# Optimization experiments

Hardware: AMD Instinct MI355X
Metric: run time of the kernel (lower is better)

## Reference

```python
import jax, jax.numpy as jnp
import numpy as np

NUM_EMBEDDINGS = 1024
EMBEDDING_DIM = 64


def setup_inputs() -> dict:
    key = jax.random.key(0)
    kx, kw = jax.random.split(key)
    x = jax.random.normal(kx, (16, 4096, EMBEDDING_DIM), dtype=jnp.float32)
    # torch init: uniform(-1/K, 1/K)
    bound = 1.0 / NUM_EMBEDDINGS
    weight = jax.random.uniform(kw, (NUM_EMBEDDINGS, EMBEDDING_DIM),
                                dtype=jnp.float32, minval=-bound, maxval=bound)
    return {"x": x, "weight": weight}


def reference(x, weight):
    flat_x = x.reshape(-1, EMBEDDING_DIM)                      # [N, D]
    x_sq = jnp.sum(flat_x ** 2, axis=1, keepdims=True)
    w_sq = jnp.sum(weight ** 2, axis=1)[None, :]
    distances = x_sq - 2.0 * (flat_x @ weight.T) + w_sq
    encoding_indices = jnp.argmin(distances, axis=1)           # [N]
    quantized = weight[encoding_indices]                       # [N, D]
    e_latent_loss = jnp.mean((jax.lax.stop_gradient(quantized) - flat_x) ** 2)
    q_latent_loss = jnp.mean((quantized - jax.lax.stop_gradient(flat_x)) ** 2)
    loss = q_latent_loss + 0.25 * e_latent_loss
    # straight-through estimator
    quantized = flat_x + jax.lax.stop_gradient(quantized - flat_x)
    return quantized.reshape(x.shape), encoding_indices, loss
```

## Files before the change

kernel.cpp:

```cpp
#include <hip/hip_runtime.h>
#include <math.h>

#define EMB_D 64
#define MARGIN 6.0e-5f

typedef float  f32x4  __attribute__((ext_vector_type(4)));
typedef short  bf16x8 __attribute__((ext_vector_type(8)));

__device__ __forceinline__ unsigned short f2bf(float f) {
    unsigned int u = __float_as_uint(f);
    return (unsigned short)((u + 0x7FFFu + ((u >> 16) & 1u)) >> 16);
}
__device__ __forceinline__ float bf2f(unsigned short h) {
    return __uint_as_float(((unsigned int)h) << 16);
}

union Pack8 { ushort u[8]; bf16x8 v; uint4 q; };

__device__ __forceinline__ bf16x8 ldbf8(const unsigned short* p) {
    union { uint4 u; bf16x8 v; } c;
    c.u = *(const uint4*)p;
    return c.v;
}

__global__ __launch_bounds__(256)
void vq_prepw_kernel(const float* __restrict__ w,
                     unsigned short* __restrict__ wt_hi,
                     unsigned short* __restrict__ wt_lo,
                     float* __restrict__ wsq, float* __restrict__ loss_out,
                     int K) {
    const int i = blockIdx.x * 256 + threadIdx.x;
    if (i == 0) loss_out[0] = 0.f;
    if (i >= K * 8) return;
    const int krow = i >> 3, q = i & 7;
    const int dest = ((krow >> 6) << 9) + (((krow >> 4) & 3) << 7) + (q << 4)
                   + (krow & 15);
    const float* src = w + (size_t)krow * EMB_D + q * 8;
    Pack8 h, l;
#pragma unroll
    for (int j = 0; j < 8; ++j) {
        const float f = src[j];
        h.u[j] = f2bf(f);
        l.u[j] = f2bf(f - bf2f(h.u[j]));
    }
    ((uint4*)wt_hi)[dest] = h.q;
    ((uint4*)wt_lo)[dest] = l.q;

    if (i < K) {
        const float* wr = w + (size_t)i * EMB_D;
        float r[8];
#pragma unroll
        for (int j = 0; j < 8; ++j) r[j] = __fmul_rn(wr[j], wr[j]);
#pragma unroll
        for (int t = 1; t < 8; ++t)
#pragma unroll
            for (int j = 0; j < 8; ++j)
                r[j] = __fadd_rn(r[j], __fmul_rn(wr[t * 8 + j], wr[t * 8 + j]));
        float a = __fadd_rn(__fadd_rn(r[0], r[1]), __fadd_rn(r[2], r[3]));
        float b = __fadd_rn(__fadd_rn(r[4], r[5]), __fadd_rn(r[6], r[7]));
        wsq[i] = __fadd_rn(a, b);
    }
}

__global__ __launch_bounds__(256, 4)
void vq_screen_kernel(const float* __restrict__ x,
                      const unsigned short* __restrict__ wt_hi,
                      const unsigned short* __restrict__ wt_lo,
                      const float* __restrict__ wsq, int* __restrict__ fidx,
                      int* __restrict__ status, int* __restrict__ k2arr,
                      int K, int N) {
    const int tid  = threadIdx.x;
    const int lane = tid & 63;
    const int wave = tid >> 6;
    const int quad = lane >> 4;
    const int c16  = lane & 15;
    const int rowbase = blockIdx.x * 64 + wave * 16;

    __shared__ uint4 sh4[512];
    __shared__ uint4 sl4[512];
    __shared__ float wsq_lds[1024];
    __shared__ float M1[4][16][17], M2[4][16][17];
    __shared__ int   N1[4][16][17], N2[4][16][17];

    const float* xrow = x + (size_t)(rowbase + c16) * EMB_D + quad * 8;
    Pack8 ah0, al0, ah1, al1;
#pragma unroll
    for (int j = 0; j < 8; ++j) {
        const float f0 = xrow[j];
        ah0.u[j] = f2bf(f0); al0.u[j] = f2bf(f0 - bf2f(ah0.u[j]));
        const float f1 = xrow[32 + j];
        ah1.u[j] = f2bf(f1); al1.u[j] = f2bf(f1 - bf2f(ah1.u[j]));
    }
    const bf16x8 ahi0 = ah0.v, alo0 = al0.v, ahi1 = ah1.v, alo1 = al1.v;

    ((float4*)wsq_lds)[tid] = ((const float4*)wsq)[tid];

    float s1[4], s2[4];
    int   k1[4], k2[4];
#pragma unroll
    for (int i = 0; i < 4; ++i) {
        s1[i] = INFINITY; s2[i] = INFINITY; k1[i] = 0; k2[i] = 0;
    }

    const uint4* gh = (const uint4*)wt_hi;
    const uint4* gl = (const uint4*)wt_lo;
    uint4 ph0 = gh[tid], ph1 = gh[256 + tid];
    uint4 pl0 = gl[tid], pl1 = gl[256 + tid];

    const int nseg = K >> 6;
    for (int seg = 0; seg < nseg; ++seg) {
        sh4[tid] = ph0; sh4[256 + tid] = ph1;
        sl4[tid] = pl0; sl4[256 + tid] = pl1;
        __syncthreads();
        if (seg + 1 < nseg) {
            const int b = (seg + 1) * 512;
            ph0 = gh[b + tid]; ph1 = gh[b + 256 + tid];
            pl0 = gl[b + tid]; pl1 = gl[b + 256 + tid];
        }

#pragma unroll
        for (int s = 0; s < 4; ++s) {
            const unsigned short* shp = (const unsigned short*)sh4;
            const unsigned short* slp = (const unsigned short*)sl4;
            const bf16x8 bhi0 = ldbf8(shp + (s * 128 + lane) * 8);
            const bf16x8 bhi1 = ldbf8(shp + (s * 128 + 64 + lane) * 8);
            const bf16x8 blo0 = ldbf8(slp + (s * 128 + lane) * 8);
            const bf16x8 blo1 = ldbf8(slp + (s * 128 + 64 + lane) * 8);

            f32x4 acc0 = {0.f, 0.f, 0.f, 0.f};
            f32x4 acc1 = {0.f, 0.f, 0.f, 0.f};
            acc0 = __builtin_amdgcn_mfma_f32_16x16x32_bf16(alo0, bhi0, acc0, 0, 0, 0);
            acc1 = __builtin_amdgcn_mfma_f32_16x16x32_bf16(alo1, bhi1, acc1, 0, 0, 0);
            acc0 = __builtin_amdgcn_mfma_f32_16x16x32_bf16(ahi0, blo0, acc0, 0, 0, 0);
            acc1 = __builtin_amdgcn_mfma_f32_16x16x32_bf16(ahi1, blo1, acc1, 0, 0, 0);
            acc0 = __builtin_amdgcn_mfma_f32_16x16x32_bf16(ahi0, bhi0, acc0, 0, 0, 0);
            acc1 = __builtin_amdgcn_mfma_f32_16x16x32_bf16(ahi1, bhi1, acc1, 0, 0, 0);

            const int   kk = seg * 64 + s * 16 + c16;
            const float wq = wsq_lds[kk];
#pragma unroll
            for (int i = 0; i < 4; ++i) {
                const float sc = fmaf(-2.0f, acc0[i] + acc1[i], wq);
                const bool c1 = sc < s1[i];
                const bool c2 = sc < s2[i];
                k2[i] = c1 ? k1[i] : (c2 ? kk : k2[i]);
                k1[i] = c1 ? kk : k1[i];
                s2[i] = __builtin_amdgcn_fmed3f(sc, s1[i], s2[i]);
                s1[i] = fminf(sc, s1[i]);
            }
        }
        __syncthreads();
    }

#pragma unroll
    for (int i = 0; i < 4; ++i) {
        const int r16 = quad * 4 + i;
        M1[wave][r16][c16] = s1[i];  N1[wave][r16][c16] = k1[i];
        M2[wave][r16][c16] = s2[i];  N2[wave][r16][c16] = k2[i];
    }
    __syncthreads();
    if (lane < 16) {
        float g1 = INFINITY, g2 = INFINITY, g3 = INFINITY;
        int   gk1 = 0, gk2 = 0;
#pragma unroll
        for (int c = 0; c < 16; ++c) {
#pragma unroll
            for (int h = 0; h < 2; ++h) {
                const float s = h == 0 ? M1[wave][lane][c] : M2[wave][lane][c];
                const int   k = h == 0 ? N1[wave][lane][c] : N2[wave][lane][c];
                if (s < g1)      { g3 = g2; g2 = g1; gk2 = gk1; g1 = s; gk1 = k; }
                else if (s < g2) { g3 = g2; g2 = s; gk2 = k; }
                else if (s < g3) { g3 = s; }
            }
        }
        const int row = rowbase + lane;
        fidx[row] = gk1;
        int st = 0;
        if (g2 - g1 <= MARGIN) st = (g3 - g1 > MARGIN) ? 1 : 2;
        status[row] = st;
        if (st == 1) k2arr[row] = gk2;
    }
}

__global__ __launch_bounds__(256)
void vq_gather_kernel(const float* __restrict__ x, const float* __restrict__ w,
                      const float* __restrict__ wsq, const int* __restrict__ fidx,
                      const int* __restrict__ status, const int* __restrict__ k2arr,
                      float* __restrict__ out, float* __restrict__ loss_out,
                      int N, int K, float scale) {
    const int tid  = threadIdx.x;
    const int lane = tid & 63;
    const int wave = tid >> 6;
    __shared__ int kf[64];
    __shared__ int strow[64];
    if (tid < 64) {
        const int row = blockIdx.x * 64 + tid;
        kf[tid]    = fidx[row];
        strow[tid] = status[row];
    }
    __syncthreads();

    if (tid < 64 && strow[tid] == 1) {
        const int row = blockIdx.x * 64 + tid;
        const int ka = kf[tid], kb = k2arr[row];
        const float4* xp = (const float4*)(x + (size_t)row * EMB_D);
        const float4* wa = (const float4*)(w + (size_t)ka * EMB_D);
        const float4* wb = (const float4*)(w + (size_t)kb * EMB_D);
        float r[8];
        double aa0 = 0, aa1 = 0, aa2 = 0, aa3 = 0;
        double ab0 = 0, ab1 = 0, ab2 = 0, ab3 = 0;
#pragma unroll
        for (int q = 0; q < 16; ++q) {
            const float4 xv = xp[q], va = wa[q], vb = wb[q];
            const int j = (q & 1) * 4;
            if (q < 2) {
                r[j + 0] = __fmul_rn(xv.x, xv.x);
                r[j + 1] = __fmul_rn(xv.y, xv.y);
                r[j + 2] = __fmul_rn(xv.z, xv.z);
                r[j + 3] = __fmul_rn(xv.w, xv.w);
            } else {
                r[j + 0] = __fadd_rn(r[j + 0], __fmul_rn(xv.x, xv.x));
                r[j + 1] = __fadd_rn(r[j + 1], __fmul_rn(xv.y, xv.y));
                r[j + 2] = __fadd_rn(r[j + 2], __fmul_rn(xv.z, xv.z));
                r[j + 3] = __fadd_rn(r[j + 3], __fmul_rn(xv.w, xv.w));
            }
            aa0 = fma((double)xv.x, (double)va.x, aa0);
            aa1 = fma((double)xv.y, (double)va.y, aa1);
            aa2 = fma((double)xv.z, (double)va.z, aa2);
            aa3 = fma((double)xv.w, (double)va.w, aa3);
            ab0 = fma((double)xv.x, (double)vb.x, ab0);
            ab1 = fma((double)xv.y, (double)vb.y, ab1);
            ab2 = fma((double)xv.z, (double)vb.z, ab2);
            ab3 = fma((double)xv.w, (double)vb.w, ab3);
        }
        const float xsq = __fadd_rn(
            __fadd_rn(__fadd_rn(r[0], r[1]), __fadd_rn(r[2], r[3])),
            __fadd_rn(__fadd_rn(r[4], r[5]), __fadd_rn(r[6], r[7])));
        const float mfa = (float)((aa0 + aa1) + (aa2 + aa3));
        const float mfb = (float)((ab0 + ab1) + (ab2 + ab3));
        const float sa = __fadd_rn(__fsub_rn(xsq, __fmul_rn(2.0f, mfa)), wsq[ka]);
        const float sb = __fadd_rn(__fsub_rn(xsq, __fmul_rn(2.0f, mfb)), wsq[kb]);
        int win = ka;
        if (sb < sa || (sb == sa && kb < ka)) win = kb;
        kf[tid] = win;
    }
    __syncthreads();

    __shared__ float4 xs4[16];
    __shared__ float  xsqs;
    __shared__ float  ls[256];
    __shared__ int    lk[256];
    for (int i = 0; i < 64; ++i) {
        if (strow[i] != 2) continue;
        const int row = blockIdx.x * 64 + i;
        if (tid < 16) xs4[tid] = ((const float4*)(x + (size_t)row * EMB_D))[tid];
        __syncthreads();
        if (tid == 0) {
            const float* xf = (const float*)xs4;
            float r[8];
#pragma unroll
            for (int j = 0; j < 8; ++j) r[j] = __fmul_rn(xf[j], xf[j]);
#pragma unroll
            for (int t = 1; t < 8; ++t)
#pragma unroll
                for (int j = 0; j < 8; ++j)
                    r[j] = __fadd_rn(r[j], __fmul_rn(xf[t * 8 + j], xf[t * 8 + j]));
            xsqs = __fadd_rn(
                __fadd_rn(__fadd_rn(r[0], r[1]), __fadd_rn(r[2], r[3])),
                __fadd_rn(__fadd_rn(r[4], r[5]), __fadd_rn(r[6], r[7])));
        }
        __syncthreads();
        const float xsq = xsqs;

        float bs = INFINITY;
        int   bk = K;
        for (int t = 0; t < 4; ++t) {
            const int k = wave * (K >> 2) + t * 64 + lane;
            const float4* wr4 = (const float4*)(w + (size_t)k * EMB_D);
            double a0 = 0.0, a1 = 0.0, a2 = 0.0, a3 = 0.0;
#pragma unroll
            for (int q = 0; q < EMB_D / 4; ++q) {
                const float4 xv = xs4[q];
                const float4 wv = wr4[q];
                a0 = fma((double)xv.x, (double)wv.x, a0);
                a1 = fma((double)xv.y, (double)wv.y, a1);
                a2 = fma((double)xv.z, (double)wv.z, a2);
                a3 = fma((double)xv.w, (double)wv.w, a3);
            }
            const float mf = (float)((a0 + a1) + (a2 + a3));
            const float t2 = __fsub_rn(xsq, __fmul_rn(2.0f, mf));
            const float sc = __fadd_rn(t2, wsq[k]);
            if (sc < bs || (sc == bs && k < bk)) { bs = sc; bk = k; }
        }
        ls[tid] = bs; lk[tid] = bk;
        __syncthreads();
        if (wave == 0) {
            float gs = ls[lane];
            int   gk = lk[lane];
#pragma unroll
            for (int c = 1; c < 4; ++c) {
                const float os = ls[c * 64 + lane];
                const int   ok = lk[c * 64 + lane];
                if (os < gs || (os == gs && ok < gk)) { gs = os; gk = ok; }
            }
#pragma unroll
            for (int off = 32; off > 0; off >>= 1) {
                const float os = __shfl_down(gs, off);
                const int   ok = __shfl_down(gk, off);
                if (os < gs || (os == gs && ok < gk)) { gs = os; gk = ok; }
            }
            if (lane == 0) kf[i] = gk;
        }
        __syncthreads();
    }

    if (tid < 64) {
        const int row = blockIdx.x * 64 + tid;
        out[(size_t)N * EMB_D + row] = (float)kf[tid];
    }
    float lpart = 0.f;
#pragma unroll
    for (int rep = 0; rep < 4; ++rep) {
        int f4   = rep * 256 + tid;
        int rr   = f4 >> 4;
        int c    = f4 & 15;
        int k    = kf[rr];
        int grow = blockIdx.x * 64 + rr;
        float4 wv = ((const float4*)(w + (size_t)k * EMB_D))[c];
        float4 xq = ((const float4*)(x + (size_t)grow * EMB_D))[c];
        ((float4*)out)[(size_t)grow * (EMB_D / 4) + c] = wv;
        float dx = wv.x - xq.x, dy = wv.y - xq.y;
        float dz = wv.z - xq.z, dw = wv.w - xq.w;
        lpart += dx * dx + dy * dy + dz * dz + dw * dw;
    }
#pragma unroll
    for (int off = 32; off > 0; off >>= 1) lpart += __shfl_down(lpart, off);
    __shared__ float lred[4];
    if (lane == 0) lred[wave] = lpart;
    __syncthreads();
    if (tid == 0)
        atomicAdd(loss_out, ((lred[0] + lred[1]) + (lred[2] + lred[3])) * scale);
}

extern "C" void kernel_launch(void* const* d_in, const int* in_sizes, int n_in,
                              void* d_out, int out_size, void* d_ws, size_t ws_size,
                              hipStream_t stream) {
    const float* x = (const float*)d_in[0];
    const float* w = (const float*)d_in[1];
    float* out = (float*)d_out;
    const int xsz = in_sizes[0];
    const int wsz = in_sizes[1];
    const int N   = xsz / EMB_D;
    const int K   = wsz / EMB_D;
    const int NB  = N / 64;
    float* loss_out = out + (size_t)N * EMB_D + N;

    int*   status = (int*)d_ws;
    int*   k2arr  = status + N;
    int*   fidx   = k2arr + N;
    float* wsq    = (float*)(fidx + N);
    unsigned short* wt_hi = (unsigned short*)(wsq + K);
    unsigned short* wt_lo = wt_hi + (size_t)K * EMB_D;

    vq_prepw_kernel<<<(K * 8 + 255) / 256, 256, 0, stream>>>(w, wt_hi, wt_lo,
                                                             wsq, loss_out, K);
    vq_screen_kernel<<<NB, 256, 0, stream>>>(x, wt_hi, wt_lo, wsq, fidx,
                                             status, k2arr, K, N);
    vq_gather_kernel<<<NB, 256, 0, stream>>>(x, w, wsq, fidx, status, k2arr,
                                             out, loss_out, N, K,
                                             1.25f / (float)xsz);
}
```

Measured before the change: 147.6 us.

## Fuse screen and gather kernels and pack score plus index into one key

Merges the screening and gather kernels into one kernel, so fidx/status/k2 are passed through shared memory and no longer round-trip through global memory, and one launch is removed. The top-2 tracking now packs a positively-offset score (with its low 10 mantissa bits truncated) together with the code index into a single unsigned key and uses integer min/max. This shortens the per-candidate compare-select chain. The truncation costs score precision, and the tie margin is widened to compensate. The key trick assumes K≤1024 and that the offset scores are positive.

```diff
diff --git a/kernel.cpp b/kernel.cpp
--- a/kernel.cpp
+++ b/kernel.cpp
@@ -2,7 +2,7 @@
 #include <math.h>
 
 #define EMB_D 64
-#define MARGIN 6.0e-5f
+#define MARGIN 1.0e-4f
 
 typedef float  f32x4  __attribute__((ext_vector_type(4)));
 typedef short  bf16x8 __attribute__((ext_vector_type(8)));
@@ -14,9 +14,7 @@
 __device__ __forceinline__ float bf2f(unsigned short h) {
     return __uint_as_float(((unsigned int)h) << 16);
 }
-
 union Pack8 { ushort u[8]; bf16x8 v; uint4 q; };
-
 __device__ __forceinline__ bf16x8 ldbf8(const unsigned short* p) {
     union { uint4 u; bf16x8 v; } c;
     c.u = *(const uint4*)p;
@@ -63,12 +61,11 @@
 }
 
 __global__ __launch_bounds__(256, 4)
-void vq_screen_kernel(const float* __restrict__ x,
-                      const unsigned short* __restrict__ wt_hi,
-                      const unsigned short* __restrict__ wt_lo,
-                      const float* __restrict__ wsq, int* __restrict__ fidx,
-                      int* __restrict__ status, int* __restrict__ k2arr,
-                      int K, int N) {
+void vq_mega_kernel(const float* __restrict__ x, const float* __restrict__ w,
+                    const unsigned short* __restrict__ wt_hi,
+                    const unsigned short* __restrict__ wt_lo,
+                    const float* __restrict__ wsq, float* __restrict__ out,
+                    float* __restrict__ loss_out, int K, int N, float scale) {
     const int tid  = threadIdx.x;
     const int lane = tid & 63;
     const int wave = tid >> 6;
@@ -78,9 +75,9 @@
 
     __shared__ uint4 sh4[512];
     __shared__ uint4 sl4[512];
-    __shared__ float wsq_lds[1024];
-    __shared__ float M1[4][16][17], M2[4][16][17];
-    __shared__ int   N1[4][16][17], N2[4][16][17];
+    __shared__ float wsqo[1024];
+    __shared__ unsigned int U1[4][16][17], U2[4][16][17];
+    __shared__ int kf[64], strow[64], k2s[64];
 
     const float* xrow = x + (size_t)(rowbase + c16) * EMB_D + quad * 8;
     Pack8 ah0, al0, ah1, al1;
@@ -93,14 +90,15 @@
     }
     const bf16x8 ahi0 = ah0.v, alo0 = al0.v, ahi1 = ah1.v, alo1 = al1.v;
 
-    ((float4*)wsq_lds)[tid] = ((const float4*)wsq)[tid];
-
-    float s1[4], s2[4];
-    int   k1[4], k2[4];
-#pragma unroll
-    for (int i = 0; i < 4; ++i) {
-        s1[i] = INFINITY; s2[i] = INFINITY; k1[i] = 0; k2[i] = 0;
-    }
+    {
+        float4 v = ((const float4*)wsq)[tid];
+        v.x += 0.25f; v.y += 0.25f; v.z += 0.25f; v.w += 0.25f;
+        ((float4*)wsqo)[tid] = v;
+    }
+
+    unsigned int u1[4], u2[4];
+#pragma unroll
+    for (int i = 0; i < 4; ++i) { u1[i] = 0xFFFFFFFFu; u2[i] = 0xFFFFFFFFu; }
 
     const uint4* gh = (const uint4*)wt_hi;
     const uint4* gl = (const uint4*)wt_lo;
@@ -117,11 +115,11 @@
             ph0 = gh[b + tid]; ph1 = gh[b + 256 + tid];
             pl0 = gl[b + tid]; pl1 = gl[b + 256 + tid];
         }
+        const unsigned short* shp = (const unsigned short*)sh4;
+        const unsigned short* slp = (const unsigned short*)sl4;
 
 #pragma unroll
         for (int s = 0; s < 4; ++s) {
-            const unsigned short* shp = (const unsigned short*)sh4;
-            const unsigned short* slp = (const unsigned short*)sl4;
             const bf16x8 bhi0 = ldbf8(shp + (s * 128 + lane) * 8);
             const bf16x8 bhi1 = ldbf8(shp + (s * 128 + 64 + lane) * 8);
             const bf16x8 blo0 = ldbf8(slp + (s * 128 + lane) * 8);
@@ -136,17 +134,16 @@
             acc0 = __builtin_amdgcn_mfma_f32_16x16x32_bf16(ahi0, bhi0, acc0, 0, 0, 0);
             acc1 = __builtin_amdgcn_mfma_f32_16x16x32_bf16(ahi1, bhi1, acc1, 0, 0, 0);
 
-            const int   kk = seg * 64 + s * 16 + c16;
-            const float wq = wsq_lds[kk];
+            const int   kk  = seg * 64 + s * 16 + c16;
+            const float wqo = wsqo[kk];
 #pragma unroll
             for (int i = 0; i < 4; ++i) {
-                const float sc = fmaf(-2.0f, acc0[i] + acc1[i], wq);
-                const bool c1 = sc < s1[i];
-                const bool c2 = sc < s2[i];
-                k2[i] = c1 ? k1[i] : (c2 ? kk : k2[i]);
-                k1[i] = c1 ? kk : k1[i];
-                s2[i] = __builtin_amdgcn_fmed3f(sc, s1[i], s2[i]);
-                s1[i] = fminf(sc, s1[i]);
+                const float sp  = fmaf(-2.0f, acc0[i] + acc1[i], wqo);
+                const unsigned int key =
+                    (__float_as_uint(sp) & 0xFFFFFC00u) | (unsigned int)kk;
+                const unsigned int mx = u1[i] > key ? u1[i] : key;
+                u1[i] = u1[i] < key ? u1[i] : key;
+                u2[i] = u2[i] < mx  ? u2[i] : mx;
             }
         }
         __syncthreads();
@@ -155,54 +152,42 @@
 #pragma unroll
     for (int i = 0; i < 4; ++i) {
         const int r16 = quad * 4 + i;
-        M1[wave][r16][c16] = s1[i];  N1[wave][r16][c16] = k1[i];
-        M2[wave][r16][c16] = s2[i];  N2[wave][r16][c16] = k2[i];
+        U1[wave][r16][c16] = u1[i];
+        U2[wave][r16][c16] = u2[i];
     }
     __syncthreads();
     if (lane < 16) {
-        float g1 = INFINITY, g2 = INFINITY, g3 = INFINITY;
-        int   gk1 = 0, gk2 = 0;
+        unsigned int g1 = 0xFFFFFFFFu, g2 = 0xFFFFFFFFu, g3 = 0xFFFFFFFFu;
 #pragma unroll
         for (int c = 0; c < 16; ++c) {
 #pragma unroll
             for (int h = 0; h < 2; ++h) {
-                const float s = h == 0 ? M1[wave][lane][c] : M2[wave][lane][c];
-                const int   k = h == 0 ? N1[wave][lane][c] : N2[wave][lane][c];
-                if (s < g1)      { g3 = g2; g2 = g1; gk2 = gk1; g1 = s; gk1 = k; }
-                else if (s < g2) { g3 = g2; g2 = s; gk2 = k; }
-                else if (s < g3) { g3 = s; }
-            }
-        }
-        const int row = rowbase + lane;
-        fidx[row] = gk1;
+                const unsigned int key = h == 0 ? U1[wave][lane][c]
+                                                : U2[wave][lane][c];
+                const unsigned int a = g1 < key ? g1 : key;
+                const unsigned int b = g1 < key ? key : g1;
+                g1 = a;
+                const unsigned int cc = g2 < b ? g2 : b;
+                const unsigned int d  = g2 < b ? b : g2;
+                g2 = cc;
+                g3 = g3 < d ? g3 : d;
+            }
+        }
+        const float s1f = __uint_as_float(g1 & 0xFFFFFC00u);
+        const float s2f = __uint_as_float(g2 & 0xFFFFFC00u);
+        const float s3f = __uint_as_float(g3 & 0xFFFFFC00u);
+        const int idx = wave * 16 + lane;
+        kf[idx]  = (int)(g1 & 1023u);
+        k2s[idx] = (int)(g2 & 1023u);
         int st = 0;
-        if (g2 - g1 <= MARGIN) st = (g3 - g1 > MARGIN) ? 1 : 2;
-        status[row] = st;
-        if (st == 1) k2arr[row] = gk2;
-    }
-}
-
-__global__ __launch_bounds__(256)
-void vq_gather_kernel(const float* __restrict__ x, const float* __restrict__ w,
-                      const float* __restrict__ wsq, const int* __restrict__ fidx,
-                      const int* __restrict__ status, const int* __restrict__ k2arr,
-                      float* __restrict__ out, float* __restrict__ loss_out,
-                      int N, int K, float scale) {
-    const int tid  = threadIdx.x;
-    const int lane = tid & 63;
-    const int wave = tid >> 6;
-    __shared__ int kf[64];
-    __shared__ int strow[64];
-    if (tid < 64) {
-        const int row = blockIdx.x * 64 + tid;
-        kf[tid]    = fidx[row];
-        strow[tid] = status[row];
+        if (s2f - s1f <= MARGIN) st = (s3f - s1f > MARGIN) ? 1 : 2;
+        strow[idx] = st;
     }
     __syncthreads();
 
     if (tid < 64 && strow[tid] == 1) {
         const int row = blockIdx.x * 64 + tid;
-        const int ka = kf[tid], kb = k2arr[row];
+        const int ka = kf[tid], kb = k2s[tid];
         const float4* xp = (const float4*)(x + (size_t)row * EMB_D);
         const float4* wa = (const float4*)(w + (size_t)ka * EMB_D);
         const float4* wb = (const float4*)(w + (size_t)kb * EMB_D);
@@ -355,18 +340,12 @@
     const int NB  = N / 64;
     float* loss_out = out + (size_t)N * EMB_D + N;
 
-    int*   status = (int*)d_ws;
-    int*   k2arr  = status + N;
-    int*   fidx   = k2arr + N;
-    float* wsq    = (float*)(fidx + N);
+    float* wsq = (float*)d_ws;
     unsigned short* wt_hi = (unsigned short*)(wsq + K);
     unsigned short* wt_lo = wt_hi + (size_t)K * EMB_D;
 
     vq_prepw_kernel<<<(K * 8 + 255) / 256, 256, 0, stream>>>(w, wt_hi, wt_lo,
                                                              wsq, loss_out, K);
-    vq_screen_kernel<<<NB, 256, 0, stream>>>(x, wt_hi, wt_lo, wsq, fidx,
-                                             status, k2arr, K, N);
-    vq_gather_kernel<<<NB, 256, 0, stream>>>(x, w, wsq, fidx, status, k2arr,
-                                             out, loss_out, N, K,
-                                             1.25f / (float)xsz);
-}
+    vq_mega_kernel<<<NB, 256, 0, stream>>>(x, w, wt_hi, wt_lo, wsq, out,
+                                           loss_out, K, N, 1.25f / (float)xsz);
+}
```

After: 167.1 us. 13.2% more time.
